# Performance work log

Measured on AMD Instinct MI355X. Metric: run time of the kernel, lower is better.

Reference implementation:

```python
import jax, jax.numpy as jnp
import numpy as np


def _bilinear_align_corners(img, H, W):
    """Bilinear resize of img [B,K,h,w] to [B,K,H,W], align_corners=True."""
    h, w = img.shape[-2], img.shape[-1]
    ys = jnp.linspace(0.0, h - 1.0, H)
    xs = jnp.linspace(0.0, w - 1.0, W)
    y0 = jnp.clip(jnp.floor(ys).astype(jnp.int32), 0, h - 1)
    y1 = jnp.minimum(y0 + 1, h - 1)
    x0 = jnp.clip(jnp.floor(xs).astype(jnp.int32), 0, w - 1)
    x1 = jnp.minimum(x0 + 1, w - 1)
    wy = (ys - y0.astype(img.dtype))[:, None]   # [H,1]
    wx = (xs - x0.astype(img.dtype))            # [W]
    r0 = img[:, :, y0, :]                        # [B,K,H,w]
    r1 = img[:, :, y1, :]
    top = r0[..., x0] * (1.0 - wx) + r0[..., x1] * wx   # [B,K,H,W]
    bot = r1[..., x0] * (1.0 - wx) + r1[..., x1] * wx
    return top * (1.0 - wy) + bot * wy


def setup_inputs() -> dict:
    key = jax.random.key(0)
    k1, k2, k3 = jax.random.split(key, 3)
    B, C, h, w = 8, 256, 64, 64
    H, W = 512, 512
    K = 21
    feature_map = jax.random.normal(k1, (B, C, h, w), dtype=jnp.float32)
    x = jax.random.uniform(k2, (B, 3, H, W), dtype=jnp.float32)
    W_cls = jax.random.normal(k3, (K, C), dtype=jnp.float32) * 0.02
    b_cls = jnp.zeros((K,), dtype=jnp.float32)
    return {"feature_map": feature_map, "x": x, "W_cls": W_cls, "b_cls": b_cls}


def reference(feature_map, x, W_cls, b_cls):
    # 1x1 conv == channel contraction
    logits = jnp.einsum('bchw,kc->bkhw', feature_map, W_cls) + b_cls[None, :, None, None]
    seg = jax.nn.softmax(logits, axis=1)                      # [B,K,h,w]
    H, W = x.shape[2], x.shape[3]
    seg = _bilinear_align_corners(seg, H, W)                  # [B,K,H,W]
    xi = jnp.transpose(x, (0, 2, 3, 1))                       # [B,H,W,3]
    # q[b,k,c] = mean over (H,W) of x * seg_k  (the per-class loop, fused)
    q = jnp.einsum('bhwc,bkhw->bkc', xi, seg) / (H * W)       # [B,K,3]
    # attn[b,k,h,w] = sum_c x[b,h,w,c] * q[b,k,c]
    segments_by_color = jnp.einsum('bhwc,bkc->bkhw', xi, q)   # [B,K,H,W]
    return segments_by_color
```

## Files before the change

kernel.cpp:

```cpp
#include <hip/hip_runtime.h>
#include <math.h>

#define NB 8
#define NC 256
#define HS 64
#define WSM 64
#define HL 512
#define WL 512
#define NK 21
#define PS (HS*WSM)
#define PL (HL*WL)

#define WT_ELEMS (NK*NC)

typedef float fx4 __attribute__((ext_vector_type(4)));


__global__ __launch_bounds__(256) void k_fused(
    const float* __restrict__ fm, const float* __restrict__ Wc,
    const float* __restrict__ bc, const float* __restrict__ x,
    float* __restrict__ qpart)
{
    int id = blockIdx.x;
    int swz = (id & 7) * 64 + (id >> 3);
    int b = swz >> 6;
    int h = swz & 63;
    int lane = threadIdx.x & 63;
    int wv   = threadIdx.x >> 6;
    int p = h * 64 + lane;

    __shared__ float sWt[NC*22];
    __shared__ float tmp[3][WL];
    __shared__ float sA[3][64];
    __shared__ float red[4][NK][64];

    for (int i = threadIdx.x; i < WT_ELEMS; i += 256) {
        int k = i >> 8;
        int c = i & 255;
        sWt[c*22 + k] = Wc[i];
    }

    const float scale = 63.0f / 511.0f;
    const float inv_scale = 511.0f / 63.0f;

    if (wv < 3) {
        int Ylo = max(0,    (int)floorf((h - 1) * inv_scale) - 1);
        int Yhi = min(HL-1, (int)ceilf ((h + 1) * inv_scale) + 1);
        const float* xc = x + (size_t)(b*3 + wv) * PL;
        fx4 acc0 = {0.f,0.f,0.f,0.f}, acc1 = {0.f,0.f,0.f,0.f};
        for (int Y = Ylo; Y <= Yhi; ++Y) {
            float fs = Y * scale;
            int i0 = (int)fs; if (i0 > HS-1) i0 = HS-1;
            float f = fs - (float)i0;
            int i1 = min(i0 + 1, HS-1);
            float wt = (i0 == h ? 1.f - f : 0.f) + (i1 == h ? f : 0.f);
            const fx4* xr = (const fx4*)(xc + (size_t)Y * WL);
            acc0 += wt * xr[lane];
            acc1 += wt * xr[lane + 64];
        }
        fx4* t4 = (fx4*)tmp[wv];
        t4[lane]      = acc0;
        t4[lane + 64] = acc1;
        const int w_ = lane;
        int Xlo = max(0,    (int)floorf((w_ - 1) * inv_scale) - 1);
        int Xhi = min(WL-1, (int)ceilf ((w_ + 1) * inv_scale) + 1);
        float a = 0.f;
        for (int X = Xlo; X <= Xhi; ++X) {
            float fs = X * scale;
            int i0 = (int)fs; if (i0 > WSM-1) i0 = WSM-1;
            float f = fs - (float)i0;
            int i1 = min(i0 + 1, WSM-1);
            float wt = (i0 == w_ ? 1.f - f : 0.f) + (i1 == w_ ? f : 0.f);
            a = fmaf(wt, tmp[wv][X], a);
        }
        sA[wv][lane] = a;
    }

    __syncthreads();

    float part[NK];
    #pragma unroll
    for (int k = 0; k < NK; ++k) part[k] = 0.f;

    const float* fmb = fm + (size_t)b * NC * PS + (size_t)(wv * 64) * PS + p;
    #pragma unroll 8
    for (int cc = 0; cc < 64; ++cc) {
        float v = __builtin_nontemporal_load(fmb + (size_t)cc * PS);
        const float* w = sWt + (wv * 64 + cc) * 22;
        #pragma unroll
        for (int k = 0; k < NK; ++k) part[k] = fmaf(v, w[k], part[k]);
    }

    #pragma unroll
    for (int k = 0; k < NK; ++k) red[wv][k][lane] = part[k];
    __syncthreads();

    float logit[NK];
    #pragma unroll
    for (int k = 0; k < NK; ++k)
        logit[k] = bc[k] + ((red[0][k][lane] + red[1][k][lane])
                          + (red[2][k][lane] + red[3][k][lane]));

    float m = logit[0];
    #pragma unroll
    for (int k = 1; k < NK; ++k) m = fmaxf(m, logit[k]);
    float s = 0.f;
    #pragma unroll
    for (int k = 0; k < NK; ++k) { logit[k] = __expf(logit[k] - m); s += logit[k]; }
    float inv = 1.f / s;

    float a0 = sA[0][lane], a1 = sA[1][lane], a2 = sA[2][lane];

    float* qb = qpart + (size_t)(b*64 + h) * 64;
    for (int k = wv; k < NK; k += 4) {
        float sv = logit[k] * inv;
        float r0 = sv * a0, r1 = sv * a1, r2 = sv * a2;
        #pragma unroll
        for (int off = 32; off; off >>= 1) {
            r0 += __shfl_down(r0, off);
            r1 += __shfl_down(r1, off);
            r2 += __shfl_down(r2, off);
        }
        if (lane == 0) {
            qb[k*3 + 0] = r0;
            qb[k*3 + 1] = r1;
            qb[k*3 + 2] = r2;
        }
    }
}

__global__ __launch_bounds__(256) void k_out(
    const float* __restrict__ x, const float* __restrict__ qpart,
    float* __restrict__ out)
{
    __shared__ float lq[64*64];
    __shared__ float sq[NK*3];
    int tid = threadIdx.x;
    int b = blockIdx.y;

    const fx4* qp4 = (const fx4*)(qpart + (size_t)b * 64 * 64);
    fx4* lq4 = (fx4*)lq;
    #pragma unroll
    for (int j = 0; j < 4; ++j) lq4[tid + j*256] = qp4[tid + j*256];
    __syncthreads();
    if (tid < NK*3) {
        float s = 0.f;
        for (int j = 0; j < 64; ++j) s += lq[j*64 + tid];
        sq[tid] = s * (1.0f / (float)PL);
    }
    __syncthreads();

    int p4 = blockIdx.x * 256 + tid;
    const fx4* xb = (const fx4*)(x + (size_t)b * 3 * PL);
    fx4 x0 = xb[p4];
    fx4 x1 = xb[PL/4 + p4];
    fx4 x2 = xb[2*(PL/4) + p4];
    fx4* ob = (fx4*)(out + (size_t)b * NK * PL);
    #pragma unroll
    for (int k = 0; k < NK; ++k) {
        fx4 o = sq[k*3+0]*x0 + sq[k*3+1]*x1 + sq[k*3+2]*x2;
        __builtin_nontemporal_store(o, ob + (size_t)k * (PL/4) + p4);
    }
}

extern "C" void kernel_launch(void* const* d_in, const int* in_sizes, int n_in,
                              void* d_out, int out_size, void* d_ws, size_t ws_size,
                              hipStream_t stream)
{
    const float* fm = (const float*)d_in[0];
    const float* x  = (const float*)d_in[1];
    const float* Wc = (const float*)d_in[2];
    const float* bc = (const float*)d_in[3];
    float* out = (float*)d_out;

    float* qpart = (float*)d_ws;

    k_fused<<<NB*HS, 256, 0, stream>>>(fm, Wc, bc, x, qpart);
    k_out<<<dim3(PL/4/256, NB), 256, 0, stream>>>(x, qpart, out);
}
```

Measured before the change: 237.6 us.

## Merge both kernels into one cooperative kernel with a grid-wide sync

Replaces the two launches (the fused logits/softmax/q-partial kernel and the output broadcast kernel) with a single cooperative kernel of 512 blocks. Phase one computes the q partials, then a grid sync, then each block loops over the output tiles. Shared memory is reused through a union and launch bounds request 2 blocks per CU. This removes one kernel launch and the gap between the kernels, but adds a grid barrier, and the output phase now runs on only 512 persistent blocks, where the old output kernel used 2048 independent blocks. Each tile also redoes the 64-row q reduction, as before.

```diff
diff --git a/kernel.cpp b/kernel.cpp
--- a/kernel.cpp
+++ b/kernel.cpp
@@ -1,5 +1,8 @@
 #include <hip/hip_runtime.h>
+#include <hip/hip_cooperative_groups.h>
 #include <math.h>
+
+namespace cg = cooperative_groups;
 
 #define NB 8
 #define NC 256
@@ -12,154 +15,171 @@
 #define PL (HL*WL)
 
 #define WT_ELEMS (NK*NC)
+#define GRID 512
+#define NTILE (NB*(PL/4)/256)
 
 typedef float fx4 __attribute__((ext_vector_type(4)));
 
-
-__global__ __launch_bounds__(256) void k_fused(
+union SMem {
+    struct {
+        float sWt[NC*22];
+        float tmp[3][WL];
+        float sA[3][64];
+        float red[4][NK][64];
+    } f;
+    struct {
+        float lq[64*64];
+        float sq[NK*3];
+    } o;
+};
+
+__global__ __launch_bounds__(256, 2) void k_all(
     const float* __restrict__ fm, const float* __restrict__ Wc,
     const float* __restrict__ bc, const float* __restrict__ x,
-    float* __restrict__ qpart)
+    float* __restrict__ qpart, float* __restrict__ out)
 {
-    int id = blockIdx.x;
-    int swz = (id & 7) * 64 + (id >> 3);
-    int b = swz >> 6;
-    int h = swz & 63;
-    int lane = threadIdx.x & 63;
-    int wv   = threadIdx.x >> 6;
-    int p = h * 64 + lane;
-
-    __shared__ float sWt[NC*22];
-    __shared__ float tmp[3][WL];
-    __shared__ float sA[3][64];
-    __shared__ float red[4][NK][64];
-
-    for (int i = threadIdx.x; i < WT_ELEMS; i += 256) {
-        int k = i >> 8;
-        int c = i & 255;
-        sWt[c*22 + k] = Wc[i];
+    __shared__ SMem S;
+    int blk = blockIdx.x;
+    int tid = threadIdx.x;
+    int lane = tid & 63;
+    int wv   = tid >> 6;
+
+    {
+        int swz = (blk & 7) * 64 + (blk >> 3);
+        int b = swz >> 6;
+        int h = swz & 63;
+        int p = h * 64 + lane;
+
+        for (int i = tid; i < WT_ELEMS; i += 256) {
+            int k = i >> 8;
+            int c = i & 255;
+            S.f.sWt[c*22 + k] = Wc[i];
+        }
+
+        const float scale = 63.0f / 511.0f;
+        const float inv_scale = 511.0f / 63.0f;
+
+        if (wv < 3) {
+            int Ylo = max(0,    (int)floorf((h - 1) * inv_scale) - 1);
+            int Yhi = min(HL-1, (int)ceilf ((h + 1) * inv_scale) + 1);
+            const float* xc = x + (size_t)(b*3 + wv) * PL;
+            fx4 acc0 = {0.f,0.f,0.f,0.f}, acc1 = {0.f,0.f,0.f,0.f};
+            for (int Y = Ylo; Y <= Yhi; ++Y) {
+                float fs = Y * scale;
+                int i0 = (int)fs; if (i0 > HS-1) i0 = HS-1;
+                float f = fs - (float)i0;
+                int i1 = min(i0 + 1, HS-1);
+                float wt = (i0 == h ? 1.f - f : 0.f) + (i1 == h ? f : 0.f);
+                const fx4* xr = (const fx4*)(xc + (size_t)Y * WL);
+                acc0 += wt * xr[lane];
+                acc1 += wt * xr[lane + 64];
+            }
+            fx4* t4 = (fx4*)S.f.tmp[wv];
+            t4[lane]      = acc0;
+            t4[lane + 64] = acc1;
+            const int w_ = lane;
+            int Xlo = max(0,    (int)floorf((w_ - 1) * inv_scale) - 1);
+            int Xhi = min(WL-1, (int)ceilf ((w_ + 1) * inv_scale) + 1);
+            float a = 0.f;
+            for (int X = Xlo; X <= Xhi; ++X) {
+                float fs = X * scale;
+                int i0 = (int)fs; if (i0 > WSM-1) i0 = WSM-1;
+                float f = fs - (float)i0;
+                int i1 = min(i0 + 1, WSM-1);
+                float wt = (i0 == w_ ? 1.f - f : 0.f) + (i1 == w_ ? f : 0.f);
+                a = fmaf(wt, S.f.tmp[wv][X], a);
+            }
+            S.f.sA[wv][lane] = a;
+        }
+
+        __syncthreads();
+
+        float part[NK];
+        #pragma unroll
+        for (int k = 0; k < NK; ++k) part[k] = 0.f;
+
+        const float* fmb = fm + (size_t)b * NC * PS + (size_t)(wv * 64) * PS + p;
+        #pragma unroll 8
+        for (int cc = 0; cc < 64; ++cc) {
+            float v = __builtin_nontemporal_load(fmb + (size_t)cc * PS);
+            const float* w = S.f.sWt + (wv * 64 + cc) * 22;
+            #pragma unroll
+            for (int k = 0; k < NK; ++k) part[k] = fmaf(v, w[k], part[k]);
+        }
+
+        #pragma unroll
+        for (int k = 0; k < NK; ++k) S.f.red[wv][k][lane] = part[k];
+        __syncthreads();
+
+        float logit[NK];
+        #pragma unroll
+        for (int k = 0; k < NK; ++k)
+            logit[k] = bc[k] + ((S.f.red[0][k][lane] + S.f.red[1][k][lane])
+                              + (S.f.red[2][k][lane] + S.f.red[3][k][lane]));
+
+        float m = logit[0];
+        #pragma unroll
+        for (int k = 1; k < NK; ++k) m = fmaxf(m, logit[k]);
+        float s = 0.f;
+        #pragma unroll
+        for (int k = 0; k < NK; ++k) { logit[k] = __expf(logit[k] - m); s += logit[k]; }
+        float inv = 1.f / s;
+
+        float a0 = S.f.sA[0][lane], a1 = S.f.sA[1][lane], a2 = S.f.sA[2][lane];
+
+        float* qb = qpart + (size_t)(b*64 + h) * 64;
+        for (int k = wv; k < NK; k += 4) {
+            float sv = logit[k] * inv;
+            float r0 = sv * a0, r1 = sv * a1, r2 = sv * a2;
+            #pragma unroll
+            for (int off = 32; off; off >>= 1) {
+                r0 += __shfl_down(r0, off);
+                r1 += __shfl_down(r1, off);
+                r2 += __shfl_down(r2, off);
+            }
+            if (lane == 0) {
+                qb[k*3 + 0] = r0;
+                qb[k*3 + 1] = r1;
+                qb[k*3 + 2] = r2;
+            }
+        }
     }
 
-    const float scale = 63.0f / 511.0f;
-    const float inv_scale = 511.0f / 63.0f;
-
-    if (wv < 3) {
-        int Ylo = max(0,    (int)floorf((h - 1) * inv_scale) - 1);
-        int Yhi = min(HL-1, (int)ceilf ((h + 1) * inv_scale) + 1);
-        const float* xc = x + (size_t)(b*3 + wv) * PL;
-        fx4 acc0 = {0.f,0.f,0.f,0.f}, acc1 = {0.f,0.f,0.f,0.f};
-        for (int Y = Ylo; Y <= Yhi; ++Y) {
-            float fs = Y * scale;
-            int i0 = (int)fs; if (i0 > HS-1) i0 = HS-1;
-            float f = fs - (float)i0;
-            int i1 = min(i0 + 1, HS-1);
-            float wt = (i0 == h ? 1.f - f : 0.f) + (i1 == h ? f : 0.f);
-            const fx4* xr = (const fx4*)(xc + (size_t)Y * WL);
-            acc0 += wt * xr[lane];
-            acc1 += wt * xr[lane + 64];
-        }
-        fx4* t4 = (fx4*)tmp[wv];
-        t4[lane]      = acc0;
-        t4[lane + 64] = acc1;
-        const int w_ = lane;
-        int Xlo = max(0,    (int)floorf((w_ - 1) * inv_scale) - 1);
-        int Xhi = min(WL-1, (int)ceilf ((w_ + 1) * inv_scale) + 1);
-        float a = 0.f;
-        for (int X = Xlo; X <= Xhi; ++X) {
-            float fs = X * scale;
-            int i0 = (int)fs; if (i0 > WSM-1) i0 = WSM-1;
-            float f = fs - (float)i0;
-            int i1 = min(i0 + 1, WSM-1);
-            float wt = (i0 == w_ ? 1.f - f : 0.f) + (i1 == w_ ? f : 0.f);
-            a = fmaf(wt, tmp[wv][X], a);
-        }
-        sA[wv][lane] = a;
-    }
-
-    __syncthreads();
-
-    float part[NK];
-    #pragma unroll
-    for (int k = 0; k < NK; ++k) part[k] = 0.f;
-
-    const float* fmb = fm + (size_t)b * NC * PS + (size_t)(wv * 64) * PS + p;
-    #pragma unroll 8
-    for (int cc = 0; cc < 64; ++cc) {
-        float v = __builtin_nontemporal_load(fmb + (size_t)cc * PS);
-        const float* w = sWt + (wv * 64 + cc) * 22;
-        #pragma unroll
-        for (int k = 0; k < NK; ++k) part[k] = fmaf(v, w[k], part[k]);
-    }
-
-    #pragma unroll
-    for (int k = 0; k < NK; ++k) red[wv][k][lane] = part[k];
-    __syncthreads();
-
-    float logit[NK];
-    #pragma unroll
-    for (int k = 0; k < NK; ++k)
-        logit[k] = bc[k] + ((red[0][k][lane] + red[1][k][lane])
-                          + (red[2][k][lane] + red[3][k][lane]));
-
-    float m = logit[0];
-    #pragma unroll
-    for (int k = 1; k < NK; ++k) m = fmaxf(m, logit[k]);
-    float s = 0.f;
-    #pragma unroll
-    for (int k = 0; k < NK; ++k) { logit[k] = __expf(logit[k] - m); s += logit[k]; }
-    float inv = 1.f / s;
-
-    float a0 = sA[0][lane], a1 = sA[1][lane], a2 = sA[2][lane];
-
-    float* qb = qpart + (size_t)(b*64 + h) * 64;
-    for (int k = wv; k < NK; k += 4) {
-        float sv = logit[k] * inv;
-        float r0 = sv * a0, r1 = sv * a1, r2 = sv * a2;
-        #pragma unroll
-        for (int off = 32; off; off >>= 1) {
-            r0 += __shfl_down(r0, off);
-            r1 += __shfl_down(r1, off);
-            r2 += __shfl_down(r2, off);
-        }
-        if (lane == 0) {
-            qb[k*3 + 0] = r0;
-            qb[k*3 + 1] = r1;
-            qb[k*3 + 2] = r2;
-        }
-    }
-}
-
-__global__ __launch_bounds__(256) void k_out(
-    const float* __restrict__ x, const float* __restrict__ qpart,
-    float* __restrict__ out)
-{
-    __shared__ float lq[64*64];
-    __shared__ float sq[NK*3];
-    int tid = threadIdx.x;
-    int b = blockIdx.y;
-
-    const fx4* qp4 = (const fx4*)(qpart + (size_t)b * 64 * 64);
-    fx4* lq4 = (fx4*)lq;
-    #pragma unroll
-    for (int j = 0; j < 4; ++j) lq4[tid + j*256] = qp4[tid + j*256];
-    __syncthreads();
-    if (tid < NK*3) {
-        float s = 0.f;
-        for (int j = 0; j < 64; ++j) s += lq[j*64 + tid];
-        sq[tid] = s * (1.0f / (float)PL);
-    }
-    __syncthreads();
-
-    int p4 = blockIdx.x * 256 + tid;
-    const fx4* xb = (const fx4*)(x + (size_t)b * 3 * PL);
-    fx4 x0 = xb[p4];
-    fx4 x1 = xb[PL/4 + p4];
-    fx4 x2 = xb[2*(PL/4) + p4];
-    fx4* ob = (fx4*)(out + (size_t)b * NK * PL);
-    #pragma unroll
-    for (int k = 0; k < NK; ++k) {
-        fx4 o = sq[k*3+0]*x0 + sq[k*3+1]*x1 + sq[k*3+2]*x2;
-        __builtin_nontemporal_store(o, ob + (size_t)k * (PL/4) + p4);
+    __threadfence();
+    cg::this_grid().sync();
+    __threadfence();
+
+    for (int t = blk; t < NTILE; t += GRID) {
+        int b    = t >> 8;
+        int tile = t & 255;
+
+        const fx4* qp4 = (const fx4*)(qpart + (size_t)b * 64 * 64);
+        fx4* lq4 = (fx4*)S.o.lq;
+        #pragma unroll
+        for (int j = 0; j < 4; ++j) lq4[tid + j*256] = qp4[tid + j*256];
+        __syncthreads();
+        if (tid < NK*3) {
+            float s = 0.f;
+            for (int j = 0; j < 64; ++j) s += S.o.lq[j*64 + tid];
+            S.o.sq[tid] = s * (1.0f / (float)PL);
+        }
+        __syncthreads();
+
+        int p4 = tile * 256 + tid;
+        const fx4* xb = (const fx4*)(x + (size_t)b * 3 * PL);
+        fx4 x0 = xb[p4];
+        fx4 x1 = xb[PL/4 + p4];
+        fx4 x2 = xb[2*(PL/4) + p4];
+        float q0[NK*3];
+        #pragma unroll
+        for (int k = 0; k < NK*3; ++k) q0[k] = S.o.sq[k];
+        fx4* ob = (fx4*)(out + (size_t)b * NK * PL);
+        #pragma unroll
+        for (int k = 0; k < NK; ++k) {
+            fx4 o = q0[k*3+0]*x0 + q0[k*3+1]*x1 + q0[k*3+2]*x2;
+            __builtin_nontemporal_store(o, ob + (size_t)k * (PL/4) + p4);
+        }
+        __syncthreads();
     }
 }
 
@@ -172,9 +192,10 @@
     const float* Wc = (const float*)d_in[2];
     const float* bc = (const float*)d_in[3];
     float* out = (float*)d_out;
-
     float* qpart = (float*)d_ws;
 
-    k_fused<<<NB*HS, 256, 0, stream>>>(fm, Wc, bc, x, qpart);
-    k_out<<<dim3(PL/4/256, NB), 256, 0, stream>>>(x, qpart, out);
+    void* args[] = { (void*)&fm, (void*)&Wc, (void*)&bc, (void*)&x,
+                     (void*)&qpart, (void*)&out };
+    hipLaunchCooperativeKernel((const void*)k_all, dim3(GRID), dim3(256),
+                               args, 0, stream);
 }
```

Result: slower. 370.0 us (+55.7%).
